# Kernel optimization log

Hardware: AMD Instinct MI355X
Metric: run time of the kernel (lower is better)

The kernel has to match this reference:

```python
import jax, jax.numpy as jnp
import numpy as np

H = 768; R = 16; L = 3; NS = 128; NQ = 128


def setup_inputs():
    key = jax.random.key(0)
    ks = iter(jax.random.split(key, 40))
    def w(shape, s=0.02):
        return (s * jax.random.normal(next(ks), shape)).astype(jnp.float32)
    return {
        "support_features": jax.random.normal(next(ks), (NS, H), jnp.float32),
        "support_labels": jax.random.randint(next(ks), (NS,), 0, 3),
        "query_features": jax.random.normal(next(ks), (NQ, H), jnp.float32),
        "sim_w1": w((H, 2 * H)), "sim_b1": jnp.zeros((H,), jnp.float32),
        "sim_w2": w((R, H)), "sim_b2": jnp.zeros((R,), jnp.float32),
        "div_w1": w((H, 2 * H)), "div_b1": jnp.zeros((H,), jnp.float32),
        "div_w2": w((R, H)), "div_b2": jnp.zeros((R,), jnp.float32),
        "rel_w": w((L, R, H, H)), "rel_b": jnp.zeros((L, R, H), jnp.float32),
        "agg_w1": w((L, H, 2 * H)), "agg_b1": jnp.zeros((L, H), jnp.float32),
        "agg_w2": w((L, H, H)), "agg_b2": jnp.zeros((L, H), jnp.float32),
        "ln_g": jnp.ones((L, H), jnp.float32), "ln_b": jnp.zeros((L, H), jnp.float32),
        "cls_w1": w((H // 2, H)), "cls_b1": jnp.zeros((H // 2,), jnp.float32),
        "cls_w2": w((3, H // 2)), "cls_b2": jnp.zeros((3,), jnp.float32),
    }


def _symmetrize(F):
    # torch loop fills [i,j] and [j,i] with value computed from pair (min(i,j), max(i,j)); diag stays 0
    N = F.shape[0]
    idx = jnp.arange(N)
    lower = (idx[:, None] > idx[None, :])
    Fs = jnp.where(lower[:, :, None], jnp.swapaxes(F, 0, 1), F)
    off = (idx[:, None] != idx[None, :]).astype(F.dtype)
    return Fs * off[:, :, None]


def _relations(x, w1, b1, w2, b2, diversity):
    h = x.shape[1]
    wa, wb = w1[:, :h], w1[:, h:]  # split concat([a,b]) @ w1^T into two matmuls
    pa = x @ wa.T                  # [N,H], contribution of first element (x_i)
    if diversity:
        d = jnp.abs(x[:, None, :] - x[None, :, :])   # [N,N,H]
        hid = jax.nn.relu(pa[:, None, :] + d @ wb.T + b1)
    else:
        pb = x @ wb.T
        hid = jax.nn.relu(pa[:, None, :] + pb[None, :, :] + b1)
    logits = hid @ w2.T + b2       # [N,N,R]
    return _symmetrize(jax.nn.softmax(logits, axis=-1))


def _layer_norm(y, g, b):
    mu = y.mean(-1, keepdims=True)
    var = ((y - mu) ** 2).mean(-1, keepdims=True)
    return (y - mu) / jnp.sqrt(var + 1e-5) * g + b


def _prop_layer(x, C, rw, rb, aw1, ab1, aw2, ab2, g, b):
    N = x.shape[0]
    T = jnp.einsum('jh,rkh->jrk', x, rw) + rb       # per-relation transform [N,R,H]
    msg = jnp.einsum('ijr,jrk->ik', C, T) / (N - 1)  # mean over N-1 neighbors (diag of C is 0)
    comb = jnp.concatenate([x, msg], axis=-1)
    agg = jax.nn.relu(comb @ aw1.T + ab1) @ aw2.T + ab2
    return _layer_norm(agg + x, g, b)


def reference(support_features, support_labels, query_features,
              sim_w1, sim_b1, sim_w2, sim_b2,
              div_w1, div_b1, div_w2, div_b2,
              rel_w, rel_b, agg_w1, agg_b1, agg_w2, agg_b2, ln_g, ln_b,
              cls_w1, cls_b1, cls_w2, cls_b2):
    all_x = jnp.concatenate([support_features, query_features], axis=0)
    sim = _relations(all_x, sim_w1, sim_b1, sim_w2, sim_b2, diversity=False)
    div = _relations(all_x, div_w1, div_b1, div_w2, div_b2, diversity=True)
    C = (sim + div) * 0.5
    x = all_x
    for l in range(L):
        x = _prop_layer(x, C, rel_w[l], rel_b[l], agg_w1[l], agg_b1[l],
                        agg_w2[l], agg_b2[l], ln_g[l], ln_b[l])
    q = x[support_features.shape[0]:]
    preds = jax.nn.relu(q @ cls_w1.T + cls_b1) @ cls_w2.T + cls_b2  # dropout = identity (eval)
    return preds, sim, div, x
```

## Files before the change

### kernel.cpp

```cpp
#include <hip/hip_runtime.h>
#include <hip/hip_bf16.h>


typedef __attribute__((ext_vector_type(8))) short s16x8;
typedef __attribute__((ext_vector_type(4))) float f32x4;

__device__ __forceinline__ short f2bf_s(float f){
  union { __hip_bfloat16 h; short s; } u; u.h = __float2bfloat16(f); return u.s;
}
__device__ __forceinline__ float bf_s2f(short s){
  union { __hip_bfloat16 h; short s; } u; u.s = s; return __bfloat162float(u.h);
}
__device__ __forceinline__ f32x4 mfma16(s16x8 a, s16x8 b, f32x4 c){
  return __builtin_amdgcn_mfma_f32_16x16x32_bf16(a, b, c, 0, 0, 0);
}
__device__ __forceinline__ void gload16(void* lds, const void* g){
  __builtin_amdgcn_global_load_lds((const __attribute__((address_space(1))) void*)g,
                                   (__attribute__((address_space(3))) void*)lds,
                                   16, 0, 0);
}
__device__ __forceinline__ unsigned pack2bf(float lo, float hi){
  return __builtin_amdgcn_perm(__float_as_uint(hi), __float_as_uint(lo), 0x07060302u);
}
__device__ __forceinline__ s16x8 absdiff_bf(uint4 a, uint4 b){
  union { s16x8 v; unsigned u[4]; } o;
  const unsigned au[4] = {a.x,a.y,a.z,a.w}, bu[4] = {b.x,b.y,b.z,b.w};
  #pragma unroll
  for (int w = 0; w < 4; ++w){
    float lo = __uint_as_float(au[w] << 16)         - __uint_as_float(bu[w] << 16);
    float hi = __uint_as_float(au[w] & 0xffff0000u) - __uint_as_float(bu[w] & 0xffff0000u);
    o.u[w] = __builtin_amdgcn_perm(__float_as_uint(hi), __float_as_uint(lo), 0x07060302u)
             & 0x7fff7fffu;
  }
  return o.v;
}

__device__ __forceinline__ void tri_decode(int b, int& i0, int& j0){
  int jb = (int)((sqrtf(2.f*(float)b + 1.f) - 1.f)*0.5f);
  while (2*(jb+1)*(jb+2) <= b) ++jb;
  while (2*jb*(jb+1) > b) --jb;
  i0 = (b - 2*jb*(jb+1))*4;
  j0 = jb*16;
}

template<int BM, int EPI>
__global__ __launch_bounds__(256) void gemm_bt2(
    const short* __restrict__ A, int lda,
    const short* __restrict__ B, int ldb,
    float* __restrict__ Cf, short* __restrict__ Cb, int ldc,
    const float* __restrict__ bias, int K, int NT)
{
  __shared__ short As[BM*128];
  __shared__ short Bs[64*128];
  const int tid = threadIdx.x, lane = tid & 63, wid = tid >> 6;
  const int nt = blockIdx.x % NT, mt = blockIdx.x / NT;
  const int m0 = mt*BM, n0 = nt*64;
  const int wm0 = (wid>>1)*(BM/2), wn0 = (wid&1)*32;
  f32x4 acc[BM/32][2] = {};
  for (int k0 = 0; k0 < K; k0 += 128){
    if (k0) __syncthreads();
    #pragma unroll
    for (int q = 0; q < BM/16; ++q){
      const int d = (wid*(BM/16)+q)*1024 + lane*16;
      const int row = d>>8, c = d&255;
      gload16((char*)As + (wid*(BM/16)+q)*1024,
              (const char*)A + (size_t)(m0+row)*lda*2 + (size_t)k0*2 + (c ^ ((row&7)<<4)));
    }
    #pragma unroll
    for (int q = 0; q < 4; ++q){
      const int d = (wid*4+q)*1024 + lane*16;
      const int row = d>>8, c = d&255;
      gload16((char*)Bs + (wid*4+q)*1024,
              (const char*)B + (size_t)(n0+row)*ldb*2 + (size_t)k0*2 + (c ^ ((row&7)<<4)));
    }
    __syncthreads();
    #pragma unroll
    for (int kk = 0; kk < 4; ++kk){
      const int colb = (kk*32 + (lane>>4)*8)*2;
      s16x8 af[BM/32], bfv[2];
      #pragma unroll
      for (int mi = 0; mi < BM/32; ++mi){
        const int row = wm0 + mi*16 + (lane&15);
        af[mi] = *(const s16x8*)((char*)As + row*256 + (colb ^ ((row&7)<<4)));
      }
      #pragma unroll
      for (int ni = 0; ni < 2; ++ni){
        const int row = wn0 + ni*16 + (lane&15);
        bfv[ni] = *(const s16x8*)((char*)Bs + row*256 + (colb ^ ((row&7)<<4)));
      }
      #pragma unroll
      for (int mi = 0; mi < BM/32; ++mi)
        #pragma unroll
        for (int ni = 0; ni < 2; ++ni)
          acc[mi][ni] = mfma16(af[mi], bfv[ni], acc[mi][ni]);
    }
  }
  #pragma unroll
  for (int mi = 0; mi < BM/32; ++mi){
    #pragma unroll
    for (int ni = 0; ni < 2; ++ni){
      const int gcol = n0 + wn0 + ni*16 + (lane&15);
      const float bv = bias[gcol];
      #pragma unroll
      for (int r = 0; r < 4; ++r){
        const int grow = m0 + wm0 + mi*16 + (lane>>4)*4 + r;
        float v = acc[mi][ni][r] + bv;
        if (EPI == 2) v = fmaxf(v, 0.f);
        if (EPI == 3) Cf[(size_t)grow*ldc + gcol] = v;
        else          Cb[(size_t)grow*ldc + gcol] = f2bf_s(v);
      }
    }
  }
}

__global__ __launch_bounds__(256) void gemm_msg(
    const short* __restrict__ A,
    const short* __restrict__ B,
    float* __restrict__ Cf, float scale)
{
  __shared__ short As[64*64];
  __shared__ short Bs[64*64];
  const int tid = threadIdx.x, lane = tid & 63, wid = tid >> 6;
  const int mt = blockIdx.x / 12, nt = blockIdx.x % 12;
  const int m0 = mt*64, n0 = nt*64, kc0 = blockIdx.y*512;
  const int wm0 = (wid>>1)*32, wn0 = (wid&1)*32;
  f32x4 acc[2][2] = {};
  for (int s = 0; s < 8; ++s){
    const int k0 = kc0 + s*64;
    if (s) __syncthreads();
    #pragma unroll
    for (int q = 0; q < 2; ++q){
      const int d = (wid*2+q)*1024 + lane*16;
      const int row = d>>7, c = d&127;
      gload16((char*)As + (wid*2+q)*1024,
              (const char*)A + (size_t)(m0+row)*8192 + (size_t)k0*2 + (c ^ ((row&7)<<4)));
    }
    #pragma unroll
    for (int rd = 0; rd < 2; ++rd){
      int ei = rd*2048 + tid*8, kr = ei>>6, nc = ei&63;
      union { uint4 v; short s4[8]; } u;
      u.v = *(const uint4*)(B + (size_t)(k0+kr)*768 + n0 + nc);
      #pragma unroll
      for (int e = 0; e < 8; ++e)
        *(short*)((char*)Bs + (nc+e)*128 + ((kr*2) ^ (((nc+e)&7)<<4))) = u.s4[e];
    }
    __syncthreads();
    #pragma unroll
    for (int kk = 0; kk < 2; ++kk){
      const int colb = (kk*32 + (lane>>4)*8)*2;
      s16x8 af[2], bfv[2];
      #pragma unroll
      for (int mi = 0; mi < 2; ++mi){
        const int row = wm0 + mi*16 + (lane&15);
        af[mi] = *(const s16x8*)((char*)As + row*128 + (colb ^ ((row&7)<<4)));
      }
      #pragma unroll
      for (int ni = 0; ni < 2; ++ni){
        const int row = wn0 + ni*16 + (lane&15);
        bfv[ni] = *(const s16x8*)((char*)Bs + row*128 + (colb ^ ((row&7)<<4)));
      }
      #pragma unroll
      for (int mi = 0; mi < 2; ++mi)
        #pragma unroll
        for (int ni = 0; ni < 2; ++ni)
          acc[mi][ni] = mfma16(af[mi], bfv[ni], acc[mi][ni]);
    }
  }
  #pragma unroll
  for (int mi = 0; mi < 2; ++mi)
    #pragma unroll
    for (int ni = 0; ni < 2; ++ni){
      const int gcol = n0 + wn0 + ni*16 + (lane&15);
      #pragma unroll
      for (int r = 0; r < 4; ++r){
        const int grow = m0 + wm0 + mi*16 + (lane>>4)*4 + r;
        atomicAdd(&Cf[(size_t)grow*768 + gcol], acc[mi][ni][r]*scale);
      }
    }
}

__global__ __launch_bounds__(256, 4) void pairrel2(
    const short* __restrict__ xb,
    const short* __restrict__ wbdiv,
    const float* __restrict__ P2,
    const short* __restrict__ w2d_g,
    float* __restrict__ Ldp)
{
  __shared__ short Bs[256*64];
  const int tid = threadIdx.x, lane = tid & 63, wv = tid >> 6;
  const int wm = wv >> 1, wc = wv & 1;
  int i0, j0; tri_decode(blockIdx.x, i0, j0);
  const int nt = blockIdx.y, n0 = nt*256;

  const short* xjp = xb + (size_t)(j0 + (lane&15))*1536 + (lane>>4)*8;
  const short* xi0p = xb + (size_t)(i0 + wm*2    )*1536 + (lane>>4)*8;
  const short* xi1p = xb + (size_t)(i0 + wm*2 + 1)*1536 + (lane>>4)*8;

  f32x4 acc[2][8] = {};
  for (int t = 0; t < 12; ++t){
    if (t) __syncthreads();
    #pragma unroll
    for (int q = 0; q < 8; ++q){
      const int d = (wv*8+q)*1024 + lane*16;
      const int row = d>>7, c = d&127;
      gload16((char*)Bs + (wv*8+q)*1024,
              (const char*)wbdiv + (size_t)(n0+row)*1536 + (size_t)t*128 + (c ^ ((row&7)<<4)));
    }
    uint4 uja  = *(const uint4*)(xjp  + t*64);
    uint4 ujb  = *(const uint4*)(xjp  + t*64 + 32);
    uint4 ui0a = *(const uint4*)(xi0p + t*64);
    uint4 ui0b = *(const uint4*)(xi0p + t*64 + 32);
    uint4 ui1a = *(const uint4*)(xi1p + t*64);
    uint4 ui1b = *(const uint4*)(xi1p + t*64 + 32);
    __syncthreads();
    #pragma unroll
    for (int kk = 0; kk < 2; ++kk){
      s16x8 af0 = absdiff_bf(kk ? ujb : uja, kk ? ui0b : ui0a);
      s16x8 af1 = absdiff_bf(kk ? ujb : uja, kk ? ui1b : ui1a);
      const int colb = (kk*32 + (lane>>4)*8)*2;
      s16x8 bfv[8];
      #pragma unroll
      for (int ni = 0; ni < 8; ++ni){
        const int row = wc*128 + ni*16 + (lane&15);
        bfv[ni] = *(const s16x8*)((char*)Bs + row*128 + (colb ^ ((row&7)<<4)));
      }
      #pragma unroll
      for (int ni = 0; ni < 8; ++ni){
        acc[0][ni] = mfma16(af0, bfv[ni], acc[0][ni]);
        acc[1][ni] = mfma16(af1, bfv[ni], acc[1][ni]);
      }
    }
  }
  __syncthreads();
  #pragma unroll
  for (int mi = 0; mi < 2; ++mi){
    #pragma unroll
    for (int ni = 0; ni < 8; ++ni){
      const int col = wc*128 + ni*16 + (lane&15);
      const float pav = P2[(size_t)(i0 + wm*2 + mi)*2304 + 1536 + n0 + col];
      #pragma unroll
      for (int r = 0; r < 4; ++r){
        const int row = wm*32 + mi*16 + (lane>>4)*4 + r;
        const float v = fmaxf(acc[mi][ni][r] + pav, 0.f);
        *(short*)((char*)Bs + row*512 + ((col*2) ^ ((row&7)<<4))) =
            (short)(__float_as_uint(v) >> 16);
      }
    }
  }
  __syncthreads();
  f32x4 acc2 = {0.f,0.f,0.f,0.f};
  const int arow = wv*16 + (lane&15);
  #pragma unroll
  for (int q = 0; q < 8; ++q){
    const int colb = (q*32 + (lane>>4)*8)*2;
    s16x8 a = *(const s16x8*)((const char*)Bs + arow*512 + (colb ^ ((arow&7)<<4)));
    s16x8 w = *(const s16x8*)(w2d_g + (size_t)(lane&15)*768 + n0 + q*32 + (lane>>4)*8);
    acc2 = mfma16(a, w, acc2);
  }
  const int r_ = lane & 15;
  #pragma unroll
  for (int r = 0; r < 4; ++r){
    const int p = wv*16 + (lane>>4)*4 + r;
    const int i = i0 + (p>>4), j = j0 + (p&15);
    Ldp[(size_t)nt*1048576 + (((size_t)i<<8) + j)*16 + r_] = acc2[r];
  }
}

__global__ __launch_bounds__(256) void simpart(
    const float* __restrict__ P2,
    const short* __restrict__ w2s_g,
    float* __restrict__ Ls)
{
  __shared__ short Hs[64*256];
  const int tid = threadIdx.x, lane = tid & 63, wv = tid >> 6;
  int i0, j0; tri_decode(blockIdx.x, i0, j0);
  const int arow = wv*16 + (lane&15);
  f32x4 acc2 = {0.f,0.f,0.f,0.f};
  for (int nt = 0; nt < 3; ++nt){
    const int n0 = nt*256;
    if (nt) __syncthreads();
    {
      const int row = tid>>2, c0 = (tid&3)*64;
      const float* pap = P2 + (size_t)(i0 + (row>>4))*2304 + n0 + c0;
      const float* pbp = P2 + (size_t)(j0 + (row&15))*2304 + 768 + n0 + c0;
      #pragma unroll
      for (int cc = 0; cc < 64; cc += 8){
        float4 a0 = *(const float4*)(pap+cc), a1 = *(const float4*)(pap+cc+4);
        float4 q0 = *(const float4*)(pbp+cc), q1 = *(const float4*)(pbp+cc+4);
        uint4 o;
        o.x = pack2bf(fmaxf(a0.x+q0.x,0.f), fmaxf(a0.y+q0.y,0.f));
        o.y = pack2bf(fmaxf(a0.z+q0.z,0.f), fmaxf(a0.w+q0.w,0.f));
        o.z = pack2bf(fmaxf(a1.x+q1.x,0.f), fmaxf(a1.y+q1.y,0.f));
        o.w = pack2bf(fmaxf(a1.z+q1.z,0.f), fmaxf(a1.w+q1.w,0.f));
        *(uint4*)((char*)Hs + row*512 + (((c0+cc)*2) ^ ((row&7)<<4))) = o;
      }
    }
    __syncthreads();
    #pragma unroll
    for (int q = 0; q < 8; ++q){
      const int colb = (q*32 + (lane>>4)*8)*2;
      s16x8 a = *(const s16x8*)((const char*)Hs + arow*512 + (colb ^ ((arow&7)<<4)));
      s16x8 w = *(const s16x8*)(w2s_g + (size_t)(lane&15)*768 + n0 + q*32 + (lane>>4)*8);
      acc2 = mfma16(a, w, acc2);
    }
  }
  const int r_ = lane & 15;
  #pragma unroll
  for (int r = 0; r < 4; ++r){
    const int p = wv*16 + (lane>>4)*4 + r;
    const int i = i0 + (p>>4), j = j0 + (p&15);
    Ls[(((size_t)i<<8) + j)*16 + r_] = acc2[r];
  }
}

__global__ __launch_bounds__(256) void finisher2(
    const float* __restrict__ Ls, const float* __restrict__ Ldp,
    const float* __restrict__ b2s, const float* __restrict__ b2d,
    float* __restrict__ simo, float* __restrict__ divo, short* __restrict__ Cb)
{
  const int p = blockIdx.x*256 + threadIdx.x;
  const int i = p >> 8, j = p & 255;
  float so[16], dd[16];
  if (i == j){
    #pragma unroll
    for (int r = 0; r < 16; ++r){ so[r] = 0.f; dd[r] = 0.f; }
  } else {
    const int si = i < j ? i : j, sj = i < j ? j : i;
    const size_t base = (((size_t)si << 8) + sj) * 16;
    float mx = -1e30f, sum;
    #pragma unroll
    for (int r = 0; r < 16; ++r){ so[r] = Ls[base+r] + b2s[r]; mx = fmaxf(mx, so[r]); }
    sum = 0.f;
    #pragma unroll
    for (int r = 0; r < 16; ++r){ so[r] = expf(so[r]-mx); sum += so[r]; }
    sum = 1.f/sum;
    #pragma unroll
    for (int r = 0; r < 16; ++r) so[r] *= sum;
    mx = -1e30f;
    #pragma unroll
    for (int r = 0; r < 16; ++r){
      dd[r] = Ldp[base+r] + Ldp[base+r+1048576] + Ldp[base+r+2097152] + b2d[r];
      mx = fmaxf(mx, dd[r]);
    }
    sum = 0.f;
    #pragma unroll
    for (int r = 0; r < 16; ++r){ dd[r] = expf(dd[r]-mx); sum += dd[r]; }
    sum = 1.f/sum;
    #pragma unroll
    for (int r = 0; r < 16; ++r) dd[r] *= sum;
  }
  const size_t ob = (size_t)p * 16;
  #pragma unroll
  for (int r = 0; r < 16; ++r){
    simo[ob+r] = so[r];
    divo[ob+r] = dd[r];
    Cb[ob+r]   = f2bf_s(0.5f*(so[r]+dd[r]));
  }
}

__global__ __launch_bounds__(512) void gemm_relT(
    const short* __restrict__ A,
    const float* __restrict__ Bf,
    short* __restrict__ T,
    const float* __restrict__ bias)
{
  __shared__ short As[256*64];
  __shared__ short Bs[64*64];
  const int tid = threadIdx.x, lane = tid & 63, wv = tid >> 6;
  const int n0 = blockIdx.x*64;
  const int wm = wv >> 1, wn = wv & 1;
  const int lswz = (lane & 7) << 4;
  const int kfrag = (lane>>4)*16;
  const int brow = tid >> 3, bc0 = (tid & 7)*8;
  int abase[4], bbase[2];
  #pragma unroll
  for (int mi = 0; mi < 4; ++mi) abase[mi] = (wm*64 + mi*16 + (lane&15))*128;
  #pragma unroll
  for (int ni = 0; ni < 2; ++ni) bbase[ni] = (wn*32 + ni*16 + (lane&15))*128;
  f32x4 acc[4][2] = {};
  for (int k0 = 0; k0 < 768; k0 += 64){
    if (k0) __syncthreads();
    #pragma unroll
    for (int q = 0; q < 4; ++q){
      const int d = wv*4096 + q*1024 + lane*16;
      const int row = d>>7, c = d&127;
      gload16((char*)As + wv*4096 + q*1024,
              (const char*)A + (size_t)row*3072 + (size_t)k0*2 + (c ^ ((row&7)<<4)));
    }
    {
      const float* bp = Bf + (size_t)(n0+brow)*768 + k0 + bc0;
      float4 v0 = *(const float4*)bp, v1 = *(const float4*)(bp+4);
      union { uint4 v; unsigned u[4]; } uo;
      uo.u[0] = pack2bf(v0.x, v0.y);
      uo.u[1] = pack2bf(v0.z, v0.w);
      uo.u[2] = pack2bf(v1.x, v1.y);
      uo.u[3] = pack2bf(v1.z, v1.w);
      *(uint4*)((char*)Bs + brow*128 + ((bc0*2) ^ ((brow&7)<<4))) = uo.v;
    }
    __syncthreads();
    #pragma unroll
    for (int kk = 0; kk < 2; ++kk){
      const int kb = (kk*64 + kfrag) ^ lswz;
      s16x8 af[4], bfv[2];
      #pragma unroll
      for (int mi = 0; mi < 4; ++mi) af[mi] = *(const s16x8*)((char*)As + abase[mi] + kb);
      #pragma unroll
      for (int ni = 0; ni < 2; ++ni) bfv[ni] = *(const s16x8*)((char*)Bs + bbase[ni] + kb);
      #pragma unroll
      for (int mi = 0; mi < 4; ++mi)
        #pragma unroll
        for (int ni = 0; ni < 2; ++ni)
          acc[mi][ni] = mfma16(af[mi], bfv[ni], acc[mi][ni]);
    }
  }
  #pragma unroll
  for (int mi = 0; mi < 4; ++mi)
    #pragma unroll
    for (int ni = 0; ni < 2; ++ni){
      const int nn = n0 + wn*32 + ni*16 + (lane&15);
      const float bv = bias[nn];
      #pragma unroll
      for (int r = 0; r < 4; ++r){
        const int row = wm*64 + mi*16 + (lane>>4)*4 + r;
        T[(size_t)row*12288 + nn] = f2bf_s(acc[mi][ni][r] + bv);
      }
    }
}

__global__ __launch_bounds__(256) void ln_kernel(
    const float* __restrict__ y, float* __restrict__ x, short* __restrict__ combx,
    const float* __restrict__ g, const float* __restrict__ b, float* __restrict__ xfinal)
{
  const int row = blockIdx.x, tid = threadIdx.x;
  float tv[3]; float s = 0.f, s2 = 0.f;
  #pragma unroll
  for (int c = 0; c < 3; ++c){
    const int idx = tid + c*256;
    const float v = y[row*768+idx] + x[row*768+idx];
    tv[c] = v; s += v; s2 += v*v;
  }
  #pragma unroll
  for (int off = 32; off > 0; off >>= 1){ s += __shfl_down(s, off); s2 += __shfl_down(s2, off); }
  __shared__ float red[8];
  const int wid = tid >> 6, lane = tid & 63;
  if (lane == 0){ red[wid] = s; red[wid+4] = s2; }
  __syncthreads();
  if (tid == 0){
    red[0] = red[0]+red[1]+red[2]+red[3];
    red[4] = red[4]+red[5]+red[6]+red[7];
  }
  __syncthreads();
  const float mu = red[0]*(1.f/768.f);
  const float var = red[4]*(1.f/768.f) - mu*mu;
  const float inv = rsqrtf(var + 1e-5f);
  #pragma unroll
  for (int c = 0; c < 3; ++c){
    const int idx = tid + c*256;
    const float v = (tv[c]-mu)*inv*g[idx] + b[idx];
    x[row*768+idx] = v;
    combx[(size_t)row*1536 + idx] = f2bf_s(v);
    if (xfinal) xfinal[row*768+idx] = v;
  }
}

__global__ void cvt_flat(const float* __restrict__ s, short* __restrict__ d, int n){
  const int i = (blockIdx.x*256 + threadIdx.x)*4;
  if (i >= n) return;
  float4 v = *(const float4*)(s+i);
  union { uint2 u; short s4[4]; } o;
  o.s4[0]=f2bf_s(v.x); o.s4[1]=f2bf_s(v.y); o.s4[2]=f2bf_s(v.z); o.s4[3]=f2bf_s(v.w);
  *(uint2*)(d+i) = o.u;
}

__global__ void cvt_w1(const float* __restrict__ sw1, const float* __restrict__ dw1,
                       short* __restrict__ dst){
  const int i = (blockIdx.x*256 + threadIdx.x)*4;
  if (i >= 2359296) return;
  const int mat = i / 589824, rem = i % 589824;
  const int r = rem / 768, c = rem % 768;
  const float* src = (mat < 2 ? sw1 : dw1) + (size_t)r*1536 + (mat&1)*768 + c;
  float4 v = *(const float4*)src;
  union { uint2 u; short s4[4]; } o;
  o.s4[0]=f2bf_s(v.x); o.s4[1]=f2bf_s(v.y); o.s4[2]=f2bf_s(v.z); o.s4[3]=f2bf_s(v.w);
  *(uint2*)(dst+i) = o.u;
}

__global__ void cvt_msg(const float* __restrict__ msgf, short* __restrict__ comb){
  const int i = (blockIdx.x*256 + threadIdx.x)*4;
  if (i >= 196608) return;
  const int row = i / 768, col = i % 768;
  float4 v = *(const float4*)(msgf + i);
  union { uint2 u; short s4[4]; } o;
  o.s4[0]=f2bf_s(v.x); o.s4[1]=f2bf_s(v.y); o.s4[2]=f2bf_s(v.z); o.s4[3]=f2bf_s(v.w);
  *(uint2*)(comb + (size_t)row*1536 + 768 + col) = o.u;
}

__global__ void concat_x(const float* __restrict__ sup, const float* __restrict__ qry,
                         float* __restrict__ xf, short* __restrict__ comb){
  const int i = (blockIdx.x*256 + threadIdx.x)*4;
  if (i >= 196608) return;
  const int row = i / 768, col = i % 768;
  const float* s = (row < 128 ? sup + (size_t)row*768 : qry + (size_t)(row-128)*768) + col;
  float4 v = *(const float4*)s;
  *(float4*)(xf+i) = v;
  union { uint2 u; short s4[4]; } o;
  o.s4[0]=f2bf_s(v.x); o.s4[1]=f2bf_s(v.y); o.s4[2]=f2bf_s(v.z); o.s4[3]=f2bf_s(v.w);
  *(uint2*)(comb + (size_t)row*1536 + col) = o.u;
}

__global__ void build_bias(const float* __restrict__ b1s, const float* __restrict__ b1d,
                           float* __restrict__ out){
  const int t = blockIdx.x*256 + threadIdx.x;
  if (t >= 2304) return;
  out[t] = (t < 768) ? b1s[t] : ((t < 1536) ? 0.f : b1d[t-1536]);
}

__global__ void cls2_kernel(const short* __restrict__ hc, const float* __restrict__ w2,
                            const float* __restrict__ b2, float* __restrict__ preds){
  const int t = blockIdx.x*192 + threadIdx.x;
  if (t >= 384) return;
  const int m = t/3, c = t - m*3;
  float s = b2[c];
  for (int k = 0; k < 384; ++k)
    s += bf_s2f(hc[m*384+k]) * w2[c*384+k];
  preds[m*3+c] = s;
}

static const size_t OFF_B1CAT = 0;
static const size_t OFF_LS    = 16384;
static const size_t OFF_MSGF  = 4210688;
static const size_t OFF_LDP   = 5242880;
static const size_t OFF_P     = 17825792;
static const size_t OFF_XF    = 20185088;
static const size_t OFF_Y     = 20971520;
static const size_t OFF_COMB  = 21757952;
static const size_t OFF_CB    = 22544384;
static const size_t OFF_W1X4  = 24641536;
static const size_t OFF_W2S   = 29360128;
static const size_t OFF_W2D   = 29384704;
static const size_t OFF_AW1   = 29409280;
static const size_t OFF_AW2   = 36487168;
static const size_t OFF_CW1   = 40026112;
static const size_t OFF_TBUF  = 40615936;
static const size_t OFF_HID1  = 46907392;
static const size_t OFF_HIDC  = 47300608;

extern "C" void kernel_launch(void* const* d_in, const int* in_sizes, int n_in,
                              void* d_out, int out_size, void* d_ws, size_t ws_size,
                              hipStream_t stream)
{
  (void)in_sizes; (void)n_in; (void)out_size; (void)ws_size;
  const float* sup    = (const float*)d_in[0];
  const float* qry    = (const float*)d_in[2];
  const float* sim_w1 = (const float*)d_in[3];
  const float* sim_b1 = (const float*)d_in[4];
  const float* sim_w2 = (const float*)d_in[5];
  const float* sim_b2 = (const float*)d_in[6];
  const float* div_w1 = (const float*)d_in[7];
  const float* div_b1 = (const float*)d_in[8];
  const float* div_w2 = (const float*)d_in[9];
  const float* div_b2 = (const float*)d_in[10];
  const float* rel_w  = (const float*)d_in[11];
  const float* rel_b  = (const float*)d_in[12];
  const float* agg_w1 = (const float*)d_in[13];
  const float* agg_b1 = (const float*)d_in[14];
  const float* agg_w2 = (const float*)d_in[15];
  const float* agg_b2 = (const float*)d_in[16];
  const float* ln_g   = (const float*)d_in[17];
  const float* ln_b   = (const float*)d_in[18];
  const float* cls_w1 = (const float*)d_in[19];
  const float* cls_b1 = (const float*)d_in[20];
  const float* cls_w2 = (const float*)d_in[21];
  const float* cls_b2 = (const float*)d_in[22];

  char* w = (char*)d_ws;
  float* B1C  = (float*)(w + OFF_B1CAT);
  float* LS   = (float*)(w + OFF_LS);
  float* MSGF = (float*)(w + OFF_MSGF);
  float* LDP  = (float*)(w + OFF_LDP);
  float* P2   = (float*)(w + OFF_P);
  float* XF   = (float*)(w + OFF_XF);
  float* Y    = (float*)(w + OFF_Y);
  short* COMB = (short*)(w + OFF_COMB);
  short* CB   = (short*)(w + OFF_CB);
  short* W1X4 = (short*)(w + OFF_W1X4);
  short* W2S  = (short*)(w + OFF_W2S);
  short* W2D  = (short*)(w + OFF_W2D);
  short* AW1  = (short*)(w + OFF_AW1);
  short* AW2  = (short*)(w + OFF_AW2);
  short* CW1  = (short*)(w + OFF_CW1);
  short* TBUF = (short*)(w + OFF_TBUF);
  short* HID1 = (short*)(w + OFF_HID1);
  short* HIDC = (short*)(w + OFF_HIDC);

  float* preds = (float*)d_out;
  float* simo  = preds + 384;
  float* divo  = simo + 1048576;
  float* xout  = divo + 1048576;

  cvt_flat<<<12,   256, 0, stream>>>(sim_w2, W2S, 12288);
  cvt_flat<<<12,   256, 0, stream>>>(div_w2, W2D, 12288);
  cvt_flat<<<3456, 256, 0, stream>>>(agg_w1, AW1, 3538944);
  cvt_flat<<<1728, 256, 0, stream>>>(agg_w2, AW2, 1769472);
  cvt_flat<<<288,  256, 0, stream>>>(cls_w1, CW1, 294912);
  cvt_w1<<<2304,   256, 0, stream>>>(sim_w1, div_w1, W1X4);
  concat_x<<<192,  256, 0, stream>>>(sup, qry, XF, COMB);
  build_bias<<<9,  256, 0, stream>>>(sim_b1, div_b1, B1C);

  gemm_bt2<64,3><<<144, 256, 0, stream>>>(COMB, 1536, W1X4, 768, P2, nullptr, 2304,
                                          B1C, 768, 36);

  pairrel2<<<dim3(544,3), 256, 0, stream>>>(COMB, W1X4 + (size_t)3*589824, P2, W2D, LDP);
  simpart<<<544, 256, 0, stream>>>(P2, W2S, LS);
  finisher2<<<256, 256, 0, stream>>>(LS, LDP, sim_b2, div_b2, simo, divo, CB);

  for (int l = 0; l < 3; ++l){
    gemm_relT<<<192, 512, 0, stream>>>(COMB, rel_w + (size_t)l*9437184, TBUF,
                                       rel_b + l*12288);
    hipMemsetAsync(MSGF, 0, 786432, stream);
    gemm_msg<<<dim3(48,8), 256, 0, stream>>>(CB, TBUF, MSGF, 1.f/255.f);
    cvt_msg<<<192, 256, 0, stream>>>(MSGF, COMB);
    gemm_bt2<32,2><<<96, 256, 0, stream>>>(COMB, 1536, AW1 + (size_t)l*1179648, 1536,
                                           nullptr, HID1, 768, agg_b1 + l*768, 1536, 12);
    gemm_bt2<32,3><<<96, 256, 0, stream>>>(HID1, 768, AW2 + (size_t)l*589824, 768,
                                           Y, nullptr, 768, agg_b2 + l*768, 768, 12);
    ln_kernel<<<256, 256, 0, stream>>>(Y, XF, COMB, ln_g + l*768, ln_b + l*768,
                                       (l == 2) ? xout : nullptr);
  }

  gemm_bt2<32,2><<<24, 256, 0, stream>>>(COMB + (size_t)128*1536, 1536, CW1, 768,
                                         nullptr, HIDC, 384, cls_b1, 768, 6);
  cls2_kernel<<<2, 192, 0, stream>>>(HIDC, cls_w2, cls_b2, preds);
}
```

Before: 349.2 us.

## Double-buffer pairrel, split-K slabs for msg, fuse setup kernels, retile GEMMs

Several independent changes. The pair-relation kernel now double-buffers its weight tiles in LDS with explicit vmcnt waits, so the next tile loads while the current one is computed. The msg GEMM writes per-K-chunk slabs that a new reduction kernel sums, which replaces the memset, atomics and convert kernel. The eight setup conversion kernels are merged into one launch. The small aggregation and classifier GEMMs use 32-wide N tiles to launch more blocks, relT is split over M with 256 threads, and abs-diff packing uses a single cvt_pk instruction. The trade-offs are more workspace, extra slab memory traffic, and lower occupancy in pairrel3.

```diff
diff --git a/kernel.cpp b/kernel.cpp
--- a/kernel.cpp
+++ b/kernel.cpp
@@ -27,10 +27,11 @@
   const unsigned au[4] = {a.x,a.y,a.z,a.w}, bu[4] = {b.x,b.y,b.z,b.w};
   #pragma unroll
   for (int w = 0; w < 4; ++w){
-    float lo = __uint_as_float(au[w] << 16)         - __uint_as_float(bu[w] << 16);
-    float hi = __uint_as_float(au[w] & 0xffff0000u) - __uint_as_float(bu[w] & 0xffff0000u);
-    o.u[w] = __builtin_amdgcn_perm(__float_as_uint(hi), __float_as_uint(lo), 0x07060302u)
-             & 0x7fff7fffu;
+    float dlo = __uint_as_float(au[w] << 16)         - __uint_as_float(bu[w] << 16);
+    float dhi = __uint_as_float(au[w] & 0xffff0000u) - __uint_as_float(bu[w] & 0xffff0000u);
+    unsigned r;
+    asm("v_cvt_pk_bf16_f32 %0, abs(%1), abs(%2)" : "=v"(r) : "v"(dlo), "v"(dhi));
+    o.u[w] = r;
   }
   return o.v;
 }
@@ -43,7 +44,7 @@
   j0 = jb*16;
 }
 
-template<int BM, int EPI>
+template<int BM, int BN, int EPI>
 __global__ __launch_bounds__(256) void gemm_bt2(
     const short* __restrict__ A, int lda,
     const short* __restrict__ B, int ldb,
@@ -51,12 +52,12 @@
     const float* __restrict__ bias, int K, int NT)
 {
   __shared__ short As[BM*128];
-  __shared__ short Bs[64*128];
+  __shared__ short Bs[BN*128];
   const int tid = threadIdx.x, lane = tid & 63, wid = tid >> 6;
   const int nt = blockIdx.x % NT, mt = blockIdx.x / NT;
-  const int m0 = mt*BM, n0 = nt*64;
-  const int wm0 = (wid>>1)*(BM/2), wn0 = (wid&1)*32;
-  f32x4 acc[BM/32][2] = {};
+  const int m0 = mt*BM, n0 = nt*BN;
+  const int wm0 = (wid>>1)*(BM/2), wn0 = (wid&1)*(BN/2);
+  f32x4 acc[BM/32][BN/32] = {};
   for (int k0 = 0; k0 < K; k0 += 128){
     if (k0) __syncthreads();
     #pragma unroll
@@ -67,38 +68,38 @@
               (const char*)A + (size_t)(m0+row)*lda*2 + (size_t)k0*2 + (c ^ ((row&7)<<4)));
     }
     #pragma unroll
-    for (int q = 0; q < 4; ++q){
-      const int d = (wid*4+q)*1024 + lane*16;
+    for (int q = 0; q < BN/16; ++q){
+      const int d = (wid*(BN/16)+q)*1024 + lane*16;
       const int row = d>>8, c = d&255;
-      gload16((char*)Bs + (wid*4+q)*1024,
+      gload16((char*)Bs + (wid*(BN/16)+q)*1024,
               (const char*)B + (size_t)(n0+row)*ldb*2 + (size_t)k0*2 + (c ^ ((row&7)<<4)));
     }
     __syncthreads();
     #pragma unroll
     for (int kk = 0; kk < 4; ++kk){
       const int colb = (kk*32 + (lane>>4)*8)*2;
-      s16x8 af[BM/32], bfv[2];
+      s16x8 af[BM/32], bfv[BN/32];
       #pragma unroll
       for (int mi = 0; mi < BM/32; ++mi){
         const int row = wm0 + mi*16 + (lane&15);
         af[mi] = *(const s16x8*)((char*)As + row*256 + (colb ^ ((row&7)<<4)));
       }
       #pragma unroll
-      for (int ni = 0; ni < 2; ++ni){
+      for (int ni = 0; ni < BN/32; ++ni){
         const int row = wn0 + ni*16 + (lane&15);
         bfv[ni] = *(const s16x8*)((char*)Bs + row*256 + (colb ^ ((row&7)<<4)));
       }
       #pragma unroll
       for (int mi = 0; mi < BM/32; ++mi)
         #pragma unroll
-        for (int ni = 0; ni < 2; ++ni)
+        for (int ni = 0; ni < BN/32; ++ni)
           acc[mi][ni] = mfma16(af[mi], bfv[ni], acc[mi][ni]);
     }
   }
   #pragma unroll
   for (int mi = 0; mi < BM/32; ++mi){
     #pragma unroll
-    for (int ni = 0; ni < 2; ++ni){
+    for (int ni = 0; ni < BN/32; ++ni){
       const int gcol = n0 + wn0 + ni*16 + (lane&15);
       const float bv = bias[gcol];
       #pragma unroll
@@ -116,7 +117,7 @@
 __global__ __launch_bounds__(256) void gemm_msg(
     const short* __restrict__ A,
     const short* __restrict__ B,
-    float* __restrict__ Cf, float scale)
+    float* __restrict__ slabs)
 {
   __shared__ short As[64*64];
   __shared__ short Bs[64*64];
@@ -166,6 +167,7 @@
           acc[mi][ni] = mfma16(af[mi], bfv[ni], acc[mi][ni]);
     }
   }
+  float* out = slabs + (size_t)blockIdx.y*196608;
   #pragma unroll
   for (int mi = 0; mi < 2; ++mi)
     #pragma unroll
@@ -174,45 +176,73 @@
       #pragma unroll
       for (int r = 0; r < 4; ++r){
         const int grow = m0 + wm0 + mi*16 + (lane>>4)*4 + r;
-        atomicAdd(&Cf[(size_t)grow*768 + gcol], acc[mi][ni][r]*scale);
-      }
-    }
-}
-
-__global__ __launch_bounds__(256, 4) void pairrel2(
+        out[(size_t)grow*768 + gcol] = acc[mi][ni][r];
+      }
+    }
+}
+
+__global__ void msgsum(const float* __restrict__ slabs, short* __restrict__ comb){
+  const int i = (blockIdx.x*256 + threadIdx.x)*4;
+  if (i >= 196608) return;
+  float4 s = {0.f,0.f,0.f,0.f};
+  #pragma unroll
+  for (int c = 0; c < 8; ++c){
+    float4 v = *(const float4*)(slabs + (size_t)c*196608 + i);
+    s.x += v.x; s.y += v.y; s.z += v.z; s.w += v.w;
+  }
+  const float sc = 1.f/255.f;
+  const int row = i/768, col = i%768;
+  union { uint2 u; short s4[4]; } o;
+  o.s4[0]=f2bf_s(s.x*sc); o.s4[1]=f2bf_s(s.y*sc);
+  o.s4[2]=f2bf_s(s.z*sc); o.s4[3]=f2bf_s(s.w*sc);
+  *(uint2*)(comb + (size_t)row*1536 + 768 + col) = o.u;
+}
+
+__device__ __forceinline__ void stageB(short* dstbase, const short* Bsrc,
+                                       int n0, int k0, int wv, int lane){
+  #pragma unroll
+  for (int q = 0; q < 8; ++q){
+    const int d = (wv*8+q)*1024 + lane*16;
+    const int row = d>>7, c = d&127;
+    gload16((char*)dstbase + (wv*8+q)*1024,
+            (const char*)Bsrc + (size_t)(n0+row)*1536 + (size_t)k0*2 + (c ^ ((row&7)<<4)));
+  }
+}
+
+__global__ __launch_bounds__(256, 2) void pairrel3(
     const short* __restrict__ xb,
     const short* __restrict__ wbdiv,
     const float* __restrict__ P2,
     const short* __restrict__ w2d_g,
     float* __restrict__ Ldp)
 {
-  __shared__ short Bs[256*64];
+  __shared__ short Bs[2*256*64];
   const int tid = threadIdx.x, lane = tid & 63, wv = tid >> 6;
   const int wm = wv >> 1, wc = wv & 1;
   int i0, j0; tri_decode(blockIdx.x, i0, j0);
   const int nt = blockIdx.y, n0 = nt*256;
 
-  const short* xjp = xb + (size_t)(j0 + (lane&15))*1536 + (lane>>4)*8;
+  const short* xjp  = xb + (size_t)(j0 + (lane&15))*1536 + (lane>>4)*8;
   const short* xi0p = xb + (size_t)(i0 + wm*2    )*1536 + (lane>>4)*8;
   const short* xi1p = xb + (size_t)(i0 + wm*2 + 1)*1536 + (lane>>4)*8;
 
+  stageB(Bs, wbdiv, n0, 0, wv, lane);
+
   f32x4 acc[2][8] = {};
   for (int t = 0; t < 12; ++t){
-    if (t) __syncthreads();
-    #pragma unroll
-    for (int q = 0; q < 8; ++q){
-      const int d = (wv*8+q)*1024 + lane*16;
-      const int row = d>>7, c = d&127;
-      gload16((char*)Bs + (wv*8+q)*1024,
-              (const char*)wbdiv + (size_t)(n0+row)*1536 + (size_t)t*128 + (c ^ ((row&7)<<4)));
-    }
+    if (t < 11) stageB(Bs + ((t+1)&1)*16384, wbdiv, n0, (t+1)*64, wv, lane);
     uint4 uja  = *(const uint4*)(xjp  + t*64);
     uint4 ujb  = *(const uint4*)(xjp  + t*64 + 32);
     uint4 ui0a = *(const uint4*)(xi0p + t*64);
     uint4 ui0b = *(const uint4*)(xi0p + t*64 + 32);
     uint4 ui1a = *(const uint4*)(xi1p + t*64);
     uint4 ui1b = *(const uint4*)(xi1p + t*64 + 32);
-    __syncthreads();
+    __builtin_amdgcn_sched_barrier(0);
+    if (t < 11) asm volatile("s_waitcnt vmcnt(8)" ::: "memory");
+    else        asm volatile("s_waitcnt vmcnt(0)" ::: "memory");
+    __builtin_amdgcn_s_barrier();
+    __builtin_amdgcn_sched_barrier(0);
+    const char* bufc = (const char*)Bs + (t&1)*32768;
     #pragma unroll
     for (int kk = 0; kk < 2; ++kk){
       s16x8 af0 = absdiff_bf(kk ? ujb : uja, kk ? ui0b : ui0a);
@@ -222,7 +252,7 @@
       #pragma unroll
       for (int ni = 0; ni < 8; ++ni){
         const int row = wc*128 + ni*16 + (lane&15);
-        bfv[ni] = *(const s16x8*)((char*)Bs + row*128 + (colb ^ ((row&7)<<4)));
+        bfv[ni] = *(const s16x8*)(bufc + row*128 + (colb ^ ((row&7)<<4)));
       }
       #pragma unroll
       for (int ni = 0; ni < 8; ++ni){
@@ -230,6 +260,8 @@
         acc[1][ni] = mfma16(af1, bfv[ni], acc[1][ni]);
       }
     }
+    __builtin_amdgcn_sched_barrier(0);
+    __builtin_amdgcn_s_barrier();
   }
   __syncthreads();
   #pragma unroll
@@ -358,54 +390,57 @@
   }
 }
 
-__global__ __launch_bounds__(512) void gemm_relT(
+__global__ __launch_bounds__(256) void gemm_relT(
     const short* __restrict__ A,
     const float* __restrict__ Bf,
     short* __restrict__ T,
     const float* __restrict__ bias)
 {
-  __shared__ short As[256*64];
+  __shared__ short As[128*64];
   __shared__ short Bs[64*64];
   const int tid = threadIdx.x, lane = tid & 63, wv = tid >> 6;
-  const int n0 = blockIdx.x*64;
+  const int nt = blockIdx.x >> 1, mt = blockIdx.x & 1;
+  const int n0 = nt*64, m0 = mt*128;
   const int wm = wv >> 1, wn = wv & 1;
-  const int lswz = (lane & 7) << 4;
-  const int kfrag = (lane>>4)*16;
-  const int brow = tid >> 3, bc0 = (tid & 7)*8;
-  int abase[4], bbase[2];
-  #pragma unroll
-  for (int mi = 0; mi < 4; ++mi) abase[mi] = (wm*64 + mi*16 + (lane&15))*128;
-  #pragma unroll
-  for (int ni = 0; ni < 2; ++ni) bbase[ni] = (wn*32 + ni*16 + (lane&15))*128;
+  const int brow = tid >> 2, q4 = tid & 3;
   f32x4 acc[4][2] = {};
   for (int k0 = 0; k0 < 768; k0 += 64){
     if (k0) __syncthreads();
     #pragma unroll
     for (int q = 0; q < 4; ++q){
-      const int d = wv*4096 + q*1024 + lane*16;
+      const int d = (wv*4+q)*1024 + lane*16;
       const int row = d>>7, c = d&127;
-      gload16((char*)As + wv*4096 + q*1024,
-              (const char*)A + (size_t)row*3072 + (size_t)k0*2 + (c ^ ((row&7)<<4)));
+      gload16((char*)As + (wv*4+q)*1024,
+              (const char*)A + (size_t)(m0+row)*3072 + (size_t)k0*2 + (c ^ ((row&7)<<4)));
     }
     {
-      const float* bp = Bf + (size_t)(n0+brow)*768 + k0 + bc0;
-      float4 v0 = *(const float4*)bp, v1 = *(const float4*)(bp+4);
-      union { uint4 v; unsigned u[4]; } uo;
-      uo.u[0] = pack2bf(v0.x, v0.y);
-      uo.u[1] = pack2bf(v0.z, v0.w);
-      uo.u[2] = pack2bf(v1.x, v1.y);
-      uo.u[3] = pack2bf(v1.z, v1.w);
-      *(uint4*)((char*)Bs + brow*128 + ((bc0*2) ^ ((brow&7)<<4))) = uo.v;
+      const float* bp = Bf + (size_t)(n0+brow)*768 + k0 + q4*16;
+      float4 v0 = *(const float4*)bp,      v1 = *(const float4*)(bp+4);
+      float4 v2 = *(const float4*)(bp+8),  v3 = *(const float4*)(bp+12);
+      union { uint4 v; unsigned u[4]; } ua, ub;
+      ua.u[0]=pack2bf(v0.x,v0.y); ua.u[1]=pack2bf(v0.z,v0.w);
+      ua.u[2]=pack2bf(v1.x,v1.y); ua.u[3]=pack2bf(v1.z,v1.w);
+      ub.u[0]=pack2bf(v2.x,v2.y); ub.u[1]=pack2bf(v2.z,v2.w);
+      ub.u[2]=pack2bf(v3.x,v3.y); ub.u[3]=pack2bf(v3.z,v3.w);
+      const int bc = q4*32;
+      *(uint4*)((char*)Bs + brow*128 + ((bc   ) ^ ((brow&7)<<4))) = ua.v;
+      *(uint4*)((char*)Bs + brow*128 + ((bc+16) ^ ((brow&7)<<4))) = ub.v;
     }
     __syncthreads();
     #pragma unroll
     for (int kk = 0; kk < 2; ++kk){
-      const int kb = (kk*64 + kfrag) ^ lswz;
+      const int kb = kk*64 + (lane>>4)*16;
       s16x8 af[4], bfv[2];
       #pragma unroll
-      for (int mi = 0; mi < 4; ++mi) af[mi] = *(const s16x8*)((char*)As + abase[mi] + kb);
-      #pragma unroll
-      for (int ni = 0; ni < 2; ++ni) bfv[ni] = *(const s16x8*)((char*)Bs + bbase[ni] + kb);
+      for (int mi = 0; mi < 4; ++mi){
+        const int row = wm*64 + mi*16 + (lane&15);
+        af[mi] = *(const s16x8*)((char*)As + row*128 + (kb ^ ((row&7)<<4)));
+      }
+      #pragma unroll
+      for (int ni = 0; ni < 2; ++ni){
+        const int row = wn*32 + ni*16 + (lane&15);
+        bfv[ni] = *(const s16x8*)((char*)Bs + row*128 + (kb ^ ((row&7)<<4)));
+      }
       #pragma unroll
       for (int mi = 0; mi < 4; ++mi)
         #pragma unroll
@@ -421,7 +456,7 @@
       const float bv = bias[nn];
       #pragma unroll
       for (int r = 0; r < 4; ++r){
-        const int row = wm*64 + mi*16 + (lane>>4)*4 + r;
+        const int row = m0 + wm*64 + mi*16 + (lane>>4)*4 + r;
         T[(size_t)row*12288 + nn] = f2bf_s(acc[mi][ni][r] + bv);
       }
     }
@@ -463,8 +498,8 @@
   }
 }
 
-__global__ void cvt_flat(const float* __restrict__ s, short* __restrict__ d, int n){
-  const int i = (blockIdx.x*256 + threadIdx.x)*4;
+__device__ __forceinline__ void cvt4(const float* __restrict__ s,
+                                     short* __restrict__ d, int i, int n){
   if (i >= n) return;
   float4 v = *(const float4*)(s+i);
   union { uint2 u; short s4[4]; } o;
@@ -472,47 +507,49 @@
   *(uint2*)(d+i) = o.u;
 }
 
-__global__ void cvt_w1(const float* __restrict__ sw1, const float* __restrict__ dw1,
-                       short* __restrict__ dst){
-  const int i = (blockIdx.x*256 + threadIdx.x)*4;
-  if (i >= 2359296) return;
-  const int mat = i / 589824, rem = i % 589824;
-  const int r = rem / 768, c = rem % 768;
-  const float* src = (mat < 2 ? sw1 : dw1) + (size_t)r*1536 + (mat&1)*768 + c;
-  float4 v = *(const float4*)src;
-  union { uint2 u; short s4[4]; } o;
-  o.s4[0]=f2bf_s(v.x); o.s4[1]=f2bf_s(v.y); o.s4[2]=f2bf_s(v.z); o.s4[3]=f2bf_s(v.w);
-  *(uint2*)(dst+i) = o.u;
-}
-
-__global__ void cvt_msg(const float* __restrict__ msgf, short* __restrict__ comb){
-  const int i = (blockIdx.x*256 + threadIdx.x)*4;
-  if (i >= 196608) return;
-  const int row = i / 768, col = i % 768;
-  float4 v = *(const float4*)(msgf + i);
-  union { uint2 u; short s4[4]; } o;
-  o.s4[0]=f2bf_s(v.x); o.s4[1]=f2bf_s(v.y); o.s4[2]=f2bf_s(v.z); o.s4[3]=f2bf_s(v.w);
-  *(uint2*)(comb + (size_t)row*1536 + 768 + col) = o.u;
-}
-
-__global__ void concat_x(const float* __restrict__ sup, const float* __restrict__ qry,
-                         float* __restrict__ xf, short* __restrict__ comb){
-  const int i = (blockIdx.x*256 + threadIdx.x)*4;
-  if (i >= 196608) return;
-  const int row = i / 768, col = i % 768;
-  const float* s = (row < 128 ? sup + (size_t)row*768 : qry + (size_t)(row-128)*768) + col;
-  float4 v = *(const float4*)s;
-  *(float4*)(xf+i) = v;
-  union { uint2 u; short s4[4]; } o;
-  o.s4[0]=f2bf_s(v.x); o.s4[1]=f2bf_s(v.y); o.s4[2]=f2bf_s(v.z); o.s4[3]=f2bf_s(v.w);
-  *(uint2*)(comb + (size_t)row*1536 + col) = o.u;
-}
-
-__global__ void build_bias(const float* __restrict__ b1s, const float* __restrict__ b1d,
-                           float* __restrict__ out){
-  const int t = blockIdx.x*256 + threadIdx.x;
-  if (t >= 2304) return;
-  out[t] = (t < 768) ? b1s[t] : ((t < 1536) ? 0.f : b1d[t-1536]);
+__global__ void setup_all(
+    const float* __restrict__ sim_w2, const float* __restrict__ div_w2,
+    const float* __restrict__ agg_w1, const float* __restrict__ agg_w2,
+    const float* __restrict__ cls_w1, const float* __restrict__ sim_w1,
+    const float* __restrict__ div_w1, const float* __restrict__ sup,
+    const float* __restrict__ qry, const float* __restrict__ sim_b1,
+    const float* __restrict__ div_b1,
+    short* __restrict__ W2S, short* __restrict__ W2D, short* __restrict__ AW1,
+    short* __restrict__ AW2, short* __restrict__ CW1, short* __restrict__ W1X4,
+    float* __restrict__ XF, short* __restrict__ COMB, float* __restrict__ B1C)
+{
+  const int b = blockIdx.x, tid = threadIdx.x;
+  if (b < 12)        cvt4(sim_w2, W2S, (b*256+tid)*4, 12288);
+  else if (b < 24)   cvt4(div_w2, W2D, ((b-12)*256+tid)*4, 12288);
+  else if (b < 3480) cvt4(agg_w1, AW1, ((b-24)*256+tid)*4, 3538944);
+  else if (b < 5208) cvt4(agg_w2, AW2, ((b-3480)*256+tid)*4, 1769472);
+  else if (b < 5496) cvt4(cls_w1, CW1, ((b-5208)*256+tid)*4, 294912);
+  else if (b < 7800){
+    const int i = ((b-5496)*256+tid)*4;
+    if (i < 2359296){
+      const int mat = i / 589824, rem = i % 589824;
+      const int r = rem / 768, c = rem % 768;
+      const float* src = (mat < 2 ? sim_w1 : div_w1) + (size_t)r*1536 + (mat&1)*768 + c;
+      float4 v = *(const float4*)src;
+      union { uint2 u; short s4[4]; } o;
+      o.s4[0]=f2bf_s(v.x); o.s4[1]=f2bf_s(v.y); o.s4[2]=f2bf_s(v.z); o.s4[3]=f2bf_s(v.w);
+      *(uint2*)(W1X4+i) = o.u;
+    }
+  } else if (b < 7992){
+    const int i = ((b-7800)*256+tid)*4;
+    if (i < 196608){
+      const int row = i / 768, col = i % 768;
+      const float* s = (row < 128 ? sup + (size_t)row*768 : qry + (size_t)(row-128)*768) + col;
+      float4 v = *(const float4*)s;
+      *(float4*)(XF+i) = v;
+      union { uint2 u; short s4[4]; } o;
+      o.s4[0]=f2bf_s(v.x); o.s4[1]=f2bf_s(v.y); o.s4[2]=f2bf_s(v.z); o.s4[3]=f2bf_s(v.w);
+      *(uint2*)(COMB + (size_t)row*1536 + col) = o.u;
+    }
+  } else {
+    for (int t = tid; t < 2304; t += 256)
+      B1C[t] = (t < 768) ? sim_b1[t] : ((t < 1536) ? 0.f : div_b1[t-1536]);
+  }
 }
 
 __global__ void cls2_kernel(const short* __restrict__ hc, const float* __restrict__ w2,
@@ -529,21 +566,21 @@
 static const size_t OFF_B1CAT = 0;
 static const size_t OFF_LS    = 16384;
 static const size_t OFF_MSGF  = 4210688;
-static const size_t OFF_LDP   = 5242880;
-static const size_t OFF_P     = 17825792;
-static const size_t OFF_XF    = 20185088;
-static const size_t OFF_Y     = 20971520;
-static const size_t OFF_COMB  = 21757952;
-static const size_t OFF_CB    = 22544384;
-static const size_t OFF_W1X4  = 24641536;
-static const size_t OFF_W2S   = 29360128;
-static const size_t OFF_W2D   = 29384704;
-static const size_t OFF_AW1   = 29409280;
-static const size_t OFF_AW2   = 36487168;
-static const size_t OFF_CW1   = 40026112;
-static const size_t OFF_TBUF  = 40615936;
-static const size_t OFF_HID1  = 46907392;
-static const size_t OFF_HIDC  = 47300608;
+static const size_t OFF_LDP   = 10502144;
+static const size_t OFF_P     = 23085056;
+static const size_t OFF_XF    = 25444352;
+static const size_t OFF_Y     = 26230784;
+static const size_t OFF_COMB  = 27017216;
+static const size_t OFF_CB    = 27803648;
+static const size_t OFF_W1X4  = 29900800;
+static const size_t OFF_W2S   = 34619392;
+static const size_t OFF_W2D   = 34643968;
+static const size_t OFF_AW1   = 34668544;
+static const size_t OFF_AW2   = 41746432;
+static const size_t OFF_CW1   = 45285376;
+static const size_t OFF_TBUF  = 45875200;
+static const size_t OFF_HID1  = 52166656;
+static const size_t OFF_HIDC  = 52559872;
 
 extern "C" void kernel_launch(void* const* d_in, const int* in_sizes, int n_in,
                               void* d_out, int out_size, void* d_ws, size_t ws_size,
@@ -598,37 +635,31 @@
   float* divo  = simo + 1048576;
   float* xout  = divo + 1048576;
 
-  cvt_flat<<<12,   256, 0, stream>>>(sim_w2, W2S, 12288);
-  cvt_flat<<<12,   256, 0, stream>>>(div_w2, W2D, 12288);
-  cvt_flat<<<3456, 256, 0, stream>>>(agg_w1, AW1, 3538944);
-  cvt_flat<<<1728, 256, 0, stream>>>(agg_w2, AW2, 1769472);
-  cvt_flat<<<288,  256, 0, stream>>>(cls_w1, CW1, 294912);
-  cvt_w1<<<2304,   256, 0, stream>>>(sim_w1, div_w1, W1X4);
-  concat_x<<<192,  256, 0, stream>>>(sup, qry, XF, COMB);
-  build_bias<<<9,  256, 0, stream>>>(sim_b1, div_b1, B1C);
-
-  gemm_bt2<64,3><<<144, 256, 0, stream>>>(COMB, 1536, W1X4, 768, P2, nullptr, 2304,
-                                          B1C, 768, 36);
-
-  pairrel2<<<dim3(544,3), 256, 0, stream>>>(COMB, W1X4 + (size_t)3*589824, P2, W2D, LDP);
+  setup_all<<<7993, 256, 0, stream>>>(sim_w2, div_w2, agg_w1, agg_w2, cls_w1,
+                                      sim_w1, div_w1, sup, qry, sim_b1, div_b1,
+                                      W2S, W2D, AW1, AW2, CW1, W1X4, XF, COMB, B1C);
+
+  gemm_bt2<64,64,3><<<144, 256, 0, stream>>>(COMB, 1536, W1X4, 768, P2, nullptr, 2304,
+                                             B1C, 768, 36);
+
+  pairrel3<<<dim3(544,3), 256, 0, stream>>>(COMB, W1X4 + (size_t)3*589824, P2, W2D, LDP);
   simpart<<<544, 256, 0, stream>>>(P2, W2S, LS);
   finisher2<<<256, 256, 0, stream>>>(LS, LDP, sim_b2, div_b2, simo, divo, CB);
 
   for (int l = 0; l < 3; ++l){
-    gemm_relT<<<192, 512, 0, stream>>>(COMB, rel_w + (size_t)l*9437184, TBUF,
+    gemm_relT<<<384, 256, 0, stream>>>(COMB, rel_w + (size_t)l*9437184, TBUF,
                                        rel_b + l*12288);
-    hipMemsetAsync(MSGF, 0, 786432, stream);
-    gemm_msg<<<dim3(48,8), 256, 0, stream>>>(CB, TBUF, MSGF, 1.f/255.f);
-    cvt_msg<<<192, 256, 0, stream>>>(MSGF, COMB);
-    gemm_bt2<32,2><<<96, 256, 0, stream>>>(COMB, 1536, AW1 + (size_t)l*1179648, 1536,
-                                           nullptr, HID1, 768, agg_b1 + l*768, 1536, 12);
-    gemm_bt2<32,3><<<96, 256, 0, stream>>>(HID1, 768, AW2 + (size_t)l*589824, 768,
-                                           Y, nullptr, 768, agg_b2 + l*768, 768, 12);
+    gemm_msg<<<dim3(48,8), 256, 0, stream>>>(CB, TBUF, MSGF);
+    msgsum<<<192, 256, 0, stream>>>(MSGF, COMB);
+    gemm_bt2<32,32,2><<<192, 256, 0, stream>>>(COMB, 1536, AW1 + (size_t)l*1179648, 1536,
+                                               nullptr, HID1, 768, agg_b1 + l*768, 1536, 24);
+    gemm_bt2<32,32,3><<<192, 256, 0, stream>>>(HID1, 768, AW2 + (size_t)l*589824, 768,
+                                               Y, nullptr, 768, agg_b2 + l*768, 768, 24);
     ln_kernel<<<256, 256, 0, stream>>>(Y, XF, COMB, ln_g + l*768, ln_b + l*768,
                                        (l == 2) ? xout : nullptr);
   }
 
-  gemm_bt2<32,2><<<24, 256, 0, stream>>>(COMB + (size_t)128*1536, 1536, CW1, 768,
-                                         nullptr, HIDC, 384, cls_b1, 768, 6);
+  gemm_bt2<32,32,2><<<48, 256, 0, stream>>>(COMB + (size_t)128*1536, 1536, CW1, 768,
+                                            nullptr, HIDC, 384, cls_b1, 768, 12);
   cls2_kernel<<<2, 192, 0, stream>>>(HIDC, cls_w2, cls_b2, preds);
 }
```

After: 320.7 us. 1.09x faster.
